# Kernel optimization log

Hardware: AMD Instinct MI355X
Metric: run time of the kernel (lower is better)

The kernel has to match this reference:

```python
import jax, jax.numpy as jnp
import numpy as np

B, L, C, S, W, R = 2, 32, 32, 64, 64, 32
MH = 32  # forcing MLP hidden


def _conv3d(x, w, b, pad_hw):
    # x: [B, Cin, L, S, W], w: [Cout, Cin, 1, kh, kw]
    y = jax.lax.conv_general_dilated(
        x, w, window_strides=(1, 1, 1),
        padding=[(0, 0), (pad_hw, pad_hw), (pad_hw, pad_hw)],
        dimension_numbers=('NCDHW', 'OIDHW', 'NCDHW'))
    return y + b[None, :, None, None, None]


def _forward(x, listT, params_log_base, dispersion_mod, fm_W1, fm_b1, fm_W2, fm_b2,
             forcing_scale, U_re, U_im, V_re, V_im, pW_re, pW_im, pb_re, pb_im,
             convr_w, convr_b, convi_w, convi_b, projc_w, projc_b, ln_w, ln_b):
    b, l, c, s, w = x.shape
    r = U_re.shape[-1]
    pad = s // 4
    dt = listT.reshape(b, l, 1, 1, 1)

    # FFT with mirror padding along S
    xp = jnp.pad(x, ((0, 0), (0, 0), (0, 0), (pad, pad), (0, 0)), mode='reflect')
    h = jnp.fft.fft2(xp.astype(jnp.complex64), axes=(-2, -1), norm='ortho')

    # complex channel projection
    proj_W = pW_re + 1j * pW_im
    h = jnp.einsum('blcsw,cd->bldsw', h, proj_W)
    h = h + (pb_re + 1j * pb_im)[None, None, :, None, None]

    # back to spatial, crop pad, re-FFT
    hs = jnp.fft.ifft2(h, axes=(-2, -1), norm='ortho')[..., pad:-pad, :]
    h = jnp.fft.fft2(hs, axes=(-2, -1), norm='ortho')

    U = U_re + 1j * U_im          # [C, S, R]
    V = V_re + 1j * V_im          # [C, W, R]
    # zq[b,l,c,r,q] = sum_{s,w} h * conj(U)[c,s,r] * V[c,w,q]
    zq = jnp.einsum('blcsw,csr,cwq->blcrq', h, jnp.conj(U), V)

    nu_base = jnp.exp(params_log_base[0] + dispersion_mod[0]).reshape(1, 1, c, r, 1)
    th_base = jnp.exp(params_log_base[1] + dispersion_mod[1]).reshape(1, 1, c, r, 1)

    # forcing modulation
    ctx = x.mean(axis=(-2, -1))                       # [B, L, C]
    inp = jnp.concatenate([ctx, dt.reshape(b, l, 1)], axis=-1)
    mid = jnp.tanh(inp @ fm_W1 + fm_b1)
    mod = (mid @ fm_W2 + fm_b2).reshape(b, l, c, r, 2)
    dnu = (forcing_scale * jnp.tanh(mod[..., 0]))[..., None]
    dth = (forcing_scale * jnp.tanh(mod[..., 1]))[..., None]

    nu_t = jnp.maximum(nu_base * dt + dnu, 1e-6)       # [B, L, C, R, 1]
    th_t = th_base * dt + dth
    lamb = jnp.exp(jax.lax.complex(-nu_t, th_t))       # complex [B, L, C, R, 1]

    gamma = jnp.sqrt(jnp.maximum(1.0 - jnp.exp(-2.0 * nu_t), 1e-12))
    x_in = zq * gamma.astype(zq.dtype)                 # [B, L, C, R, R]

    # parallel linear-recurrence scan: z_t = lamb_t * z_{t-1} + x_t
    def comb(a, bb):
        a1, x1 = a
        a2, x2 = bb
        return a1 * a2, a2 * x1 + x2
    _, z_out = jax.lax.associative_scan(comb, (lamb, x_in), axis=1)

    # reconstruct spectral field and inverse FFT
    h_rec = jnp.einsum('blcrq,cwq,csr->blcsw', z_out, jnp.conj(V), U)
    h_sp = jnp.fft.ifft2(h_rec, axes=(-2, -1), norm='ortho')

    xr = jnp.transpose(h_sp.real, (0, 2, 1, 3, 4))     # [B, C, L, S, W]
    xi = jnp.transpose(h_sp.imag, (0, 2, 1, 3, 4))
    hr = _conv3d(xr, convr_w, convr_b, 1)
    hi = _conv3d(xi, convi_w, convi_b, 1)
    hf = _conv3d(jnp.concatenate([hr, hi], axis=1), projc_w, projc_b, 0)
    hf = jnp.transpose(hf, (0, 2, 1, 3, 4))            # [B, L, C, S, W]

    # LayerNorm over [S, W]
    mu = hf.mean(axis=(-2, -1), keepdims=True)
    var = hf.var(axis=(-2, -1), keepdims=True)
    hf = (hf - mu) / jnp.sqrt(var + 1e-5) * ln_w + ln_b

    return x + hf


def setup_inputs() -> dict:
    key = jax.random.key(0)
    ks = jax.random.split(key, 20)
    f32 = jnp.float32
    x = jax.random.normal(ks[0], (B, L, C, S, W), dtype=f32)
    listT = jax.random.uniform(ks[1], (B, L), dtype=f32, minval=0.5, maxval=1.5)

    r_min, r_max = 0.8, 0.99
    u1 = jax.random.uniform(ks[2], (C, R), dtype=f32)
    u2 = jax.random.uniform(ks[3], (C, R), dtype=f32)
    nu_log = jnp.log(-0.5 * jnp.log(u1 * (r_max ** 2 - r_min ** 2) + r_min ** 2))
    theta_log = jnp.log(u2 * (2.0 * np.pi))
    params_log_base = jnp.stack([nu_log, theta_log], axis=0)
    dispersion_mod = jnp.zeros((2, C, R), dtype=f32)

    fm_W1 = jax.random.normal(ks[4], (C + 1, MH), dtype=f32) / np.sqrt(C + 1)
    fm_b1 = jnp.zeros((MH,), dtype=f32)
    fm_W2 = jax.random.normal(ks[5], (MH, C * R * 2), dtype=f32) / np.sqrt(MH)
    fm_b2 = jnp.zeros((C * R * 2,), dtype=f32)
    forcing_scale = jnp.float32(0.1)

    cplx_scale = 1.0 / np.sqrt(2.0)
    U_re = jax.random.normal(ks[6], (C, S, R), dtype=f32) * cplx_scale / np.sqrt(S)
    U_im = jax.random.normal(ks[7], (C, S, R), dtype=f32) * cplx_scale / np.sqrt(S)
    V_re = jax.random.normal(ks[8], (C, W, R), dtype=f32) * cplx_scale / np.sqrt(W)
    V_im = jax.random.normal(ks[9], (C, W, R), dtype=f32) * cplx_scale / np.sqrt(W)
    pW_re = jax.random.normal(ks[10], (C, C), dtype=f32) * cplx_scale / np.sqrt(C)
    pW_im = jax.random.normal(ks[11], (C, C), dtype=f32) * cplx_scale / np.sqrt(C)
    pb_re = jnp.zeros((C,), dtype=f32)
    pb_im = jnp.zeros((C,), dtype=f32)

    convr_w = jax.random.normal(ks[12], (C, C, 1, 3, 3), dtype=f32) * (1.0 / np.sqrt(C * 9))
    convr_b = jnp.zeros((C,), dtype=f32)
    convi_w = jax.random.normal(ks[13], (C, C, 1, 3, 3), dtype=f32) * (1.0 / np.sqrt(C * 9))
    convi_b = jnp.zeros((C,), dtype=f32)
    projc_w = jax.random.normal(ks[14], (C, 2 * C, 1, 1, 1), dtype=f32) * (1.0 / np.sqrt(2 * C))
    projc_b = jnp.zeros((C,), dtype=f32)

    ln_w = jnp.ones((S, W), dtype=f32)
    ln_b = jnp.zeros((S, W), dtype=f32)

    return dict(x=x, listT=listT, params_log_base=params_log_base,
                dispersion_mod=dispersion_mod, fm_W1=fm_W1, fm_b1=fm_b1,
                fm_W2=fm_W2, fm_b2=fm_b2, forcing_scale=forcing_scale,
                U_re=U_re, U_im=U_im, V_re=V_re, V_im=V_im,
                pW_re=pW_re, pW_im=pW_im, pb_re=pb_re, pb_im=pb_im,
                convr_w=convr_w, convr_b=convr_b, convi_w=convi_w, convi_b=convi_b,
                projc_w=projc_w, projc_b=projc_b, ln_w=ln_w, ln_b=ln_b)


def reference(x, listT, params_log_base, dispersion_mod, fm_W1, fm_b1, fm_W2, fm_b2,
              forcing_scale, U_re, U_im, V_re, V_im, pW_re, pW_im, pb_re, pb_im,
              convr_w, convr_b, convi_w, convi_b, projc_w, projc_b, ln_w, ln_b):
    return _forward(x, listT, params_log_base, dispersion_mod, fm_W1, fm_b1, fm_W2,
                    fm_b2, forcing_scale, U_re, U_im, V_re, V_im, pW_re, pW_im,
                    pb_re, pb_im, convr_w, convr_b, convi_w, convi_b, projc_w,
                    projc_b, ln_w, ln_b)
```

## Files before the change

kernel.cpp:

```cpp
#include <hip/hip_runtime.h>


typedef __attribute__((ext_vector_type(8))) short short8;
typedef __attribute__((ext_vector_type(4))) float floatx4;

__device__ __forceinline__ unsigned pack_bf16(float re, float im) {
  unsigned a = __float_as_uint(re), b = __float_as_uint(im);
  a = (a + 0x7FFFu + ((a >> 16) & 1u)) >> 16;
  b = (b + 0x7FFFu + ((b >> 16) & 1u)) >> 16;
  return a | (b << 16);
}
__device__ __forceinline__ unsigned short bf16r(float v) {
  unsigned a = __float_as_uint(v);
  return (unsigned short)((a + 0x7FFFu + ((a >> 16) & 1u)) >> 16);
}

__global__ __launch_bounds__(256) void k_mixprep(
    const float* __restrict__ x, const float* __restrict__ pWr,
    const float* __restrict__ pWi,
    const float* __restrict__ U_re, const float* __restrict__ U_im,
    const float* __restrict__ V_re, const float* __restrict__ V_im,
    const float* __restrict__ projc_w, const float* __restrict__ convr_w,
    const float* __restrict__ convi_w,
    unsigned* __restrict__ hs, float* __restrict__ ctxp,
    unsigned* __restrict__ zqA, unsigned* __restrict__ recA,
    unsigned* __restrict__ recB, unsigned* __restrict__ Wtb) {
  __shared__ __align__(16) char smem[512 * 20 * 4 + 16 * 16 * 2 * 4];
  const int tid = threadIdx.x;
  if (blockIdx.x < 512) {
    unsigned* xb_s = (unsigned*)smem;
    float(*red)[16][2] = (float(*)[16][2])(smem + 40960);
    const int bl = blockIdx.x >> 3;
    const int seg = blockIdx.x & 7;
    const int pxbase = seg * 512;
    const float* xb = x + (size_t)bl * 131072 + pxbase;
    float csa = 0.f, csb = 0.f;
#pragma unroll
    for (int t = 0; t < 8; ++t) {
      int i = t * 256 + tid;
      int c2 = i & 15, g4 = i >> 4;
      float4 a = *(const float4*)(xb + (2 * c2) * 4096 + g4 * 4);
      float4 b = *(const float4*)(xb + (2 * c2 + 1) * 4096 + g4 * 4);
      csa += a.x + a.y + a.z + a.w;
      csb += b.x + b.y + b.z + b.w;
#pragma unroll
      for (int j = 0; j < 4; ++j) {
        int px = g4 * 4 + j;
        xb_s[px * 20 + (((c2 >> 2) ^ (px & 3)) << 2) + (c2 & 3)] =
            pack_bf16(((const float*)&a)[j], ((const float*)&b)[j]);
      }
    }
    red[tid & 15][tid >> 4][0] = csa;
    red[tid & 15][tid >> 4][1] = csb;
    const int lane = tid & 63, wv = tid >> 6;
    const int qd = lane >> 4, ln = lane & 15;
    short8 arL, aiL, arH, aiH;
#pragma unroll
    for (int j = 0; j < 8; ++j) {
      int ci = qd * 8 + j;
      ((short*)&arL)[j] = (short)bf16r(pWr[ci * 32 + ln]);
      ((short*)&aiL)[j] = (short)bf16r(pWi[ci * 32 + ln]);
      ((short*)&arH)[j] = (short)bf16r(pWr[ci * 32 + 16 + ln]);
      ((short*)&aiH)[j] = (short)bf16r(pWi[ci * 32 + 16 + ln]);
    }
    __syncthreads();
    if (tid < 32) {
      int c2 = tid >> 1, part = tid & 1;
      float s = 0.f;
#pragma unroll
      for (int w = 0; w < 16; ++w) s += red[c2][w][part];
      ctxp[(bl * 8 + seg) * 32 + 2 * c2 + part] = s;
    }
#pragma unroll
    for (int pt = 0; pt < 8; ++pt) {
      int pxt = wv * 8 + pt;
      int pxl = pxt * 16 + ln;
      short8 bfr = *(const short8*)&xb_s[pxl * 20 + ((qd ^ (pxl & 3)) << 2)];
      floatx4 dRL = {0.f, 0.f, 0.f, 0.f}, dIL = {0.f, 0.f, 0.f, 0.f};
      floatx4 dRH = {0.f, 0.f, 0.f, 0.f}, dIH = {0.f, 0.f, 0.f, 0.f};
      dRL = __builtin_amdgcn_mfma_f32_16x16x32_bf16(arL, bfr, dRL, 0, 0, 0);
      dIL = __builtin_amdgcn_mfma_f32_16x16x32_bf16(aiL, bfr, dIL, 0, 0, 0);
      dRH = __builtin_amdgcn_mfma_f32_16x16x32_bf16(arH, bfr, dRH, 0, 0, 0);
      dIH = __builtin_amdgcn_mfma_f32_16x16x32_bf16(aiH, bfr, dIH, 0, 0, 0);
      unsigned* ho = hs + (size_t)bl * 131072 + pxbase + pxt * 16 + ln;
#pragma unroll
      for (int j = 0; j < 4; ++j) {
        ho[(qd * 4 + j) * 4096] = pack_bf16(dRL[j], dIL[j]);
        ho[(16 + qd * 4 + j) * 4096] = pack_bf16(dRH[j], dIH[j]);
      }
    }
  } else if (blockIdx.x < 2560) {
    float2* tw = (float2*)smem;
    if (tid < 64) {
      float sa, ca;
      sincosf((float)tid * 0.09817477042468103f, &sa, &ca);
      tw[tid] = make_float2(ca, sa);
    }
    __syncthreads();
    int gid = (blockIdx.x - 512) * 256 + tid;
    const float *Ar, *Ai;
    int knum, mode, variant;
    bool plus;
    unsigned* dst;
    int didx;
    if (gid < 262144) {
      int c = gid >> 13, mat = (gid >> 11) & 3, m = (gid >> 6) & 31,
          kw = gid & 63;
      knum = kw; mode = m;
      if (mat < 2) { Ar = V_re + c * 2048; Ai = V_im + c * 2048; plus = false; }
      else         { Ar = U_re + c * 2048; Ai = U_im + c * 2048; plus = true; }
      variant = mat; dst = zqA; didx = gid;
    } else {
      int rid = gid - 262144;
      int c = rid >> 13, sub = rid & 8191;
      int which = sub >> 11, mm = (sub >> 5) & 63, k2 = sub & 31;
      knum = mm; mode = k2;
      if (which < 2) {
        Ar = U_re + c * 2048; Ai = U_im + c * 2048; plus = true;
        variant = 4 + which; dst = recA;
        didx = ((c * 2 + which) * 64 + mm) * 32 + k2;
      } else {
        Ar = V_re + c * 2048; Ai = V_im + c * 2048; plus = false;
        variant = 4 + which; dst = recB;
        didx = ((c * 2 + which - 2) * 64 + mm) * 32 + k2;
      }
    }
    float sr = 0.f, si = 0.f;
    for (int n = 0; n < 64; ++n) {
      float2 w = tw[(knum * n) & 63];
      float ar = Ar[n * 32 + mode], ai = Ai[n * 32 + mode];
      if (plus) { sr += ar * w.x - ai * w.y; si += ar * w.y + ai * w.x; }
      else      { sr += ar * w.x + ai * w.y; si += ai * w.x - ar * w.y; }
    }
    sr *= 0.125f; si *= 0.125f;
    unsigned pv;
    switch (variant) {
      case 0: pv = pack_bf16(sr, -si); break;
      case 1: pv = pack_bf16(si, sr); break;
      case 2: pv = pack_bf16(sr, si); break;
      case 3: pv = pack_bf16(-si, sr); break;
      case 4: pv = pack_bf16(sr, -si); break;
      case 5: pv = pack_bf16(si, sr); break;
      case 6: pv = pack_bf16(sr, si); break;
      default: pv = pack_bf16(-si, sr); break;
    }
    dst[didx] = pv;
  } else {
    int gid = (blockIdx.x - 2560) * 256 + tid;
    if (gid < 9216) {
      int co = gid / 288;
      int r2 = gid - co * 288;
      int tap = r2 >> 5, ci = r2 & 31;
      float sr = 0.f, si = 0.f;
      for (int m = 0; m < 32; ++m) {
        sr += projc_w[co * 64 + m]      * convr_w[(m * 32 + ci) * 9 + tap];
        si += projc_w[co * 64 + 32 + m] * convi_w[(m * 32 + ci) * 9 + tap];
      }
      Wtb[gid] = pack_bf16(sr, si);
    }
  }
}

__global__ __launch_bounds__(256) void k_zq(
    const unsigned* __restrict__ hs, const short* __restrict__ zqA,
    float2* __restrict__ zq,
    const float* __restrict__ ctxp, const float* __restrict__ listT,
    const float* __restrict__ plb, const float* __restrict__ dmod,
    const float* __restrict__ W1, const float* __restrict__ b1,
    const float* __restrict__ W2, const float* __restrict__ b2,
    const float* __restrict__ fscale,
    float2* __restrict__ lam, float* __restrict__ gam) {
  __shared__ unsigned HsB[4096];
  __shared__ unsigned T2[2048];
  __shared__ float mid_s[32];
  __shared__ float ctxs[32];
  const int tid = threadIdx.x;
  if (blockIdx.x >= 2048) {
    int bl = blockIdx.x - 2048;
    float dt = listT[bl];
    if (tid < 32) {
      float s = 0.f;
#pragma unroll
      for (int sg = 0; sg < 8; ++sg) s += ctxp[(bl * 8 + sg) * 32 + tid];
      ctxs[tid] = s * (1.f / 4096.f);
    }
    __syncthreads();
    if (tid < 32) {
      float a = b1[tid];
      for (int j = 0; j < 32; ++j) a += ctxs[j] * W1[j * 32 + tid];
      a += dt * W1[1024 + tid];
      mid_s[tid] = tanhf(a);
    }
    __syncthreads();
    float fs = fscale[0];
#pragma unroll
    for (int u = 0; u < 4; ++u) {
      int cr = u * 256 + tid;
      int col = cr * 2;
      float m0 = b2[col], m1 = b2[col + 1];
      for (int h = 0; h < 32; ++h) {
        float mh = mid_s[h];
        float2 w2 = *(const float2*)&W2[h * 2048 + col];
        m0 += mh * w2.x;
        m1 += mh * w2.y;
      }
      float dnu = fs * tanhf(m0);
      float dth = fs * tanhf(m1);
      float nub = expf(plb[cr] + dmod[cr]);
      float thb = expf(plb[1024 + cr] + dmod[1024 + cr]);
      float nut = fmaxf(nub * dt + dnu, 1e-6f);
      float tht = thb * dt + dth;
      float e = expf(-nut);
      float sa, ca;
      sincosf(tht, &sa, &ca);
      float g = sqrtf(fmaxf(1.f - expf(-2.f * nut), 1e-12f));
      int o = bl * 1024 + cr;
      lam[o] = make_float2(e * ca, e * sa);
      gam[o] = g;
    }
    return;
  }
  const int blc = blockIdx.x;
  const int c = blc & 31;
  const int lane = tid & 63, wv = tid >> 6;
  const int qd = lane >> 4, ln = lane & 15;
  const int mt = wv >> 1, nth = wv & 1;
  {
    const uint4* hp = (const uint4*)(hs + (size_t)blc * 4096);
#pragma unroll
    for (int it = 0; it < 4; ++it) {
      int i4 = tid + it * 256;
      uint4 v = hp[i4];
      int s = i4 >> 4, w4 = i4 & 15;
      *(uint4*)&HsB[s * 64 + ((w4 ^ (s & 15)) << 2)] = v;
    }
  }
  const short* zA = zqA + (size_t)c * 4 * 32 * 128;
  short8 a1[4], a2[4], a3[4], a4[4];
#pragma unroll
  for (int t = 0; t < 4; ++t) {
    int row = mt * 16 + ln;
    a1[t] = *(const short8*)(zA + (0 * 32 + row) * 128 + t * 32 + qd * 8);
    a2[t] = *(const short8*)(zA + (1 * 32 + row) * 128 + t * 32 + qd * 8);
    a3[t] = *(const short8*)(zA + (2 * 32 + row) * 128 + t * 32 + qd * 8);
    a4[t] = *(const short8*)(zA + (3 * 32 + row) * 128 + t * 32 + qd * 8);
  }
  __syncthreads();
#pragma unroll
  for (int nti = 0; nti < 2; ++nti) {
    int nt = nth * 2 + nti;
    int n = nt * 16 + ln;
    floatx4 accr = {0.f, 0.f, 0.f, 0.f}, acci = {0.f, 0.f, 0.f, 0.f};
#pragma unroll
    for (int t = 0; t < 4; ++t) {
      short8 b = *(const short8*)&HsB[n * 64 + (((4 * t + qd) ^ (n & 15)) << 2)];
      accr = __builtin_amdgcn_mfma_f32_16x16x32_bf16(a1[t], b, accr, 0, 0, 0);
      acci = __builtin_amdgcn_mfma_f32_16x16x32_bf16(a2[t], b, acci, 0, 0, 0);
    }
#pragma unroll
    for (int j = 0; j < 4; ++j) {
      int q = mt * 16 + qd * 4 + j;
      int s = n;
      T2[q * 64 + (((s >> 2) ^ (q & 15)) << 2) + (s & 3)] = pack_bf16(accr[j], acci[j]);
    }
  }
  __syncthreads();
  {
    const int mt2 = wv >> 1, nt2 = wv & 1;
    int n = nt2 * 16 + ln;
    floatx4 zr = {0.f, 0.f, 0.f, 0.f}, zi = {0.f, 0.f, 0.f, 0.f};
#pragma unroll
    for (int t = 0; t < 4; ++t) {
      short8 b = *(const short8*)&T2[n * 64 + (((4 * t + qd) ^ (n & 15)) << 2)];
      zr = __builtin_amdgcn_mfma_f32_16x16x32_bf16(a3[t], b, zr, 0, 0, 0);
      zi = __builtin_amdgcn_mfma_f32_16x16x32_bf16(a4[t], b, zi, 0, 0, 0);
    }
    float2* zo = zq + (size_t)blc * 1024;
#pragma unroll
    for (int j = 0; j < 4; ++j) {
      int r = mt2 * 16 + qd * 4 + j;
      zo[r * 32 + n] = make_float2(zr[j], zi[j]);
    }
  }
}

__global__ __launch_bounds__(256) void k_scan(const float2* __restrict__ lam,
                                              const float* __restrict__ gam,
                                              const float2* __restrict__ zin,
                                              unsigned* __restrict__ zsp,
                                              int zst) {
  __shared__ float2 se[4][64];
  __shared__ float2 pe[4][64];
  __shared__ float2 cr_s[4][64];
  const int bc = blockIdx.x >> 4;
  const int b = bc >> 5, c = bc & 31;
  const int rq0 = (blockIdx.x & 15) * 64;
  const int seg = threadIdx.x >> 6, u = threadIdx.x & 63;
  const int rq = rq0 + u, r = rq >> 5;
  const int t0 = seg * 8;
  float2 s = make_float2(0.f, 0.f), P = make_float2(1.f, 0.f);
  float2 zloc[8], Ps[8];
  float2 v = zin[((size_t)(b * 32 + t0) * 32 + c) * 1024 + rq];
  float2 lm = lam[(b * 32 + t0) * 1024 + c * 32 + r];
  float g = gam[(b * 32 + t0) * 1024 + c * 32 + r];
#pragma unroll
  for (int i = 0; i < 8; ++i) {
    float2 nv, nlm;
    float ng;
    if (i < 7) {
      int t = t0 + i + 1;
      nv = zin[((size_t)(b * 32 + t) * 32 + c) * 1024 + rq];
      nlm = lam[(b * 32 + t) * 1024 + c * 32 + r];
      ng = gam[(b * 32 + t) * 1024 + c * 32 + r];
    }
    float nr = lm.x * s.x - lm.y * s.y + g * v.x;
    float ni = lm.x * s.y + lm.y * s.x + g * v.y;
    s = make_float2(nr, ni);
    float pr = P.x * lm.x - P.y * lm.y;
    float pi = P.x * lm.y + P.y * lm.x;
    P = make_float2(pr, pi);
    zloc[i] = s;
    Ps[i] = P;
    v = nv; lm = nlm; g = ng;
  }
  se[seg][u] = s;
  pe[seg][u] = P;
  __syncthreads();
  if (threadIdx.x < 64) {
    float2 c1 = se[0][u];
    float2 p1 = pe[1][u], s1 = se[1][u];
    float2 c2 = make_float2(s1.x + p1.x * c1.x - p1.y * c1.y,
                            s1.y + p1.x * c1.y + p1.y * c1.x);
    float2 p2 = pe[2][u], s2 = se[2][u];
    float2 c3 = make_float2(s2.x + p2.x * c2.x - p2.y * c2.y,
                            s2.y + p2.x * c2.y + p2.y * c2.x);
    cr_s[0][u] = make_float2(0.f, 0.f);
    cr_s[1][u] = c1;
    cr_s[2][u] = c2;
    cr_s[3][u] = c3;
  }
  __syncthreads();
  float2 cr = cr_s[seg][u];
#pragma unroll
  for (int i = 0; i < 8; ++i) {
    float zr = zloc[i].x + Ps[i].x * cr.x - Ps[i].y * cr.y;
    float zi = zloc[i].y + Ps[i].x * cr.y + Ps[i].y * cr.x;
    size_t idx = ((size_t)(b * 32 + t0 + i) * 32 + c) * 1024 + rq;
    zsp[idx * zst] = pack_bf16(zr, zi);
  }
}

__global__ __launch_bounds__(256) void k_rec(const unsigned* __restrict__ zs,
                                             int zst,
                                             const short* __restrict__ recA,
                                             const short* __restrict__ recB,
                                             unsigned* __restrict__ hsp) {
  __shared__ unsigned zB[1024];
  __shared__ unsigned P[2048];
  const int blc = blockIdx.x;
  const int c = blc & 31;
  const int tid = threadIdx.x;
  const int lane = tid & 63, wv = tid >> 6;
  const int qd = lane >> 4, ln = lane & 15;
  {
    const unsigned* zp = zs + (size_t)blc * 1024 * zst;
#pragma unroll
    for (int it = 0; it < 4; ++it) {
      int i = tid + it * 256;
      unsigned pv = zp[(size_t)i * zst];
      int r = i >> 5, q = i & 31;
      zB[q * 32 + (((r >> 2) ^ (q & 7)) << 2) + (r & 3)] = pv;
    }
  }
  const short* rA = recA + (size_t)c * 2 * 64 * 64;
  short8 a5[2], a6[2];
#pragma unroll
  for (int t = 0; t < 2; ++t) {
    int row = wv * 16 + ln;
    a5[t] = *(const short8*)(rA + (0 * 64 + row) * 64 + t * 32 + qd * 8);
    a6[t] = *(const short8*)(rA + (1 * 64 + row) * 64 + t * 32 + qd * 8);
  }
  __syncthreads();
#pragma unroll
  for (int nt = 0; nt < 2; ++nt) {
    int n = nt * 16 + ln;
    floatx4 pr = {0.f, 0.f, 0.f, 0.f}, pi = {0.f, 0.f, 0.f, 0.f};
#pragma unroll
    for (int t = 0; t < 2; ++t) {
      short8 b = *(const short8*)&zB[n * 32 + (((4 * t + qd) ^ (n & 7)) << 2)];
      pr = __builtin_amdgcn_mfma_f32_16x16x32_bf16(a5[t], b, pr, 0, 0, 0);
      pi = __builtin_amdgcn_mfma_f32_16x16x32_bf16(a6[t], b, pi, 0, 0, 0);
    }
#pragma unroll
    for (int j = 0; j < 4; ++j) {
      int s = wv * 16 + qd * 4 + j;
      int q = n;
      P[s * 32 + (((q >> 2) ^ (s & 7)) << 2) + (q & 3)] = pack_bf16(pr[j], pi[j]);
    }
  }
  __syncthreads();
  const short* rB = recB + (size_t)c * 2 * 64 * 64;
  short8 pa[2];
#pragma unroll
  for (int t = 0; t < 2; ++t) {
    int row = wv * 16 + ln;
    pa[t] = *(const short8*)&P[row * 32 + (((4 * t + qd) ^ (row & 7)) << 2)];
  }
#pragma unroll
  for (int nt = 0; nt < 4; ++nt) {
    int n = nt * 16 + ln;
    floatx4 hr = {0.f, 0.f, 0.f, 0.f}, hi = {0.f, 0.f, 0.f, 0.f};
#pragma unroll
    for (int t = 0; t < 2; ++t) {
      short8 b5 = *(const short8*)(rB + (0 * 64 + n) * 64 + t * 32 + qd * 8);
      short8 b6 = *(const short8*)(rB + (1 * 64 + n) * 64 + t * 32 + qd * 8);
      hr = __builtin_amdgcn_mfma_f32_16x16x32_bf16(pa[t], b5, hr, 0, 0, 0);
      hi = __builtin_amdgcn_mfma_f32_16x16x32_bf16(pa[t], b6, hi, 0, 0, 0);
    }
    unsigned* ho = hsp + (size_t)blc * 4096;
#pragma unroll
    for (int j = 0; j < 4; ++j) {
      int s = wv * 16 + qd * 4 + j;
      ho[s * 64 + n] = pack_bf16(hr[j], hi[j]);
    }
  }
}

__global__ __launch_bounds__(256, 2) void k_conv(
    const unsigned* __restrict__ hsp, const short* __restrict__ Wtb,
    unsigned short* __restrict__ convout, float2* __restrict__ stats) {
  __shared__ unsigned lds_in[6 * 66 * 32];
  const int bl = blockIdx.x >> 4;
  const int slab = blockIdx.x & 15;
  const int y0 = slab * 4;
  const int tid = threadIdx.x;
  for (int i = tid; i < 384; i += 256) {
    int ci = i & 31, j = i >> 5;
    int yi = j >> 1, xi = (j & 1) ? 65 : 0;
    int slot = (ci >> 2) ^ (xi & 7);
    lds_in[(yi * 66 + xi) * 32 + slot * 4 + (ci & 3)] = 0u;
  }
#pragma unroll
  for (int t = 0; t < 12; ++t) {
    int i = t * 256 + tid;
    int ci = i & 31;
    int j = i >> 5;
    int yi = j >> 4, x4 = j & 15;
    int y = y0 + yi - 1;
    uint4 v = make_uint4(0u, 0u, 0u, 0u);
    if ((unsigned)y < 64u)
      v = *(const uint4*)(hsp + (((size_t)bl * 32 + ci) * 64 + y) * 64 + x4 * 4);
    int xb = 1 + x4 * 4;
#pragma unroll
    for (int jj = 0; jj < 4; ++jj) {
      int xi = xb + jj;
      int slot = (ci >> 2) ^ (xi & 7);
      lds_in[(yi * 66 + xi) * 32 + slot * 4 + (ci & 3)] =
          ((const unsigned*)&v)[jj];
    }
  }
  const int lane = tid & 63;
  const int wv = tid >> 6;
  const int co = lane & 15;
  const int qd = lane >> 4;
  short8 bL[18], bH[18];
  {
    const short* wpL = Wtb + (co * 9) * 64 + qd * 8;
    const short* wpH = Wtb + ((co + 16) * 9) * 64 + qd * 8;
#pragma unroll
    for (int tap = 0; tap < 9; ++tap)
#pragma unroll
      for (int kk = 0; kk < 2; ++kk) {
        bL[tap * 2 + kk] = *(const short8*)(wpL + tap * 64 + kk * 32);
        bH[tap * 2 + kk] = *(const short8*)(wpH + tap * 64 + kk * 32);
      }
  }
  __syncthreads();
  float sL = 0.f, s2L = 0.f, sH = 0.f, s2H = 0.f;
  const int x0 = wv * 16;
  const int xl = lane & 15;
  for (int ry = 0; ry < 4; ++ry) {
    floatx4 aL = {0.f, 0.f, 0.f, 0.f}, aH = {0.f, 0.f, 0.f, 0.f};
#pragma unroll
    for (int tap = 0; tap < 9; ++tap) {
      int dy = tap / 3, dx = tap - dy * 3;
      int yi = ry + dy;
      int xi = x0 + xl + dx;
#pragma unroll
      for (int kk = 0; kk < 2; ++kk) {
        int slot = ((kk << 2) | qd) ^ (xi & 7);
        const short8 a =
            *(const short8*)&lds_in[(yi * 66 + xi) * 32 + slot * 4];
        aL = __builtin_amdgcn_mfma_f32_16x16x32_bf16(a, bL[tap * 2 + kk], aL, 0, 0, 0);
        aH = __builtin_amdgcn_mfma_f32_16x16x32_bf16(a, bH[tap * 2 + kk], aH, 0, 0, 0);
      }
    }
    size_t goL = (((size_t)bl * 32 + co) * 64 + (y0 + ry)) * 64 + x0 + qd * 4;
    size_t goH = goL + (size_t)16 * 4096;
    *(uint2*)(convout + goL) =
        make_uint2(pack_bf16(aL[0], aL[1]), pack_bf16(aL[2], aL[3]));
    *(uint2*)(convout + goH) =
        make_uint2(pack_bf16(aH[0], aH[1]), pack_bf16(aH[2], aH[3]));
#pragma unroll
    for (int j = 0; j < 4; ++j) {
      sL += aL[j]; s2L += aL[j] * aL[j];
      sH += aH[j]; s2H += aH[j] * aH[j];
    }
  }
  sL += __shfl_down(sL, 32, 64);  s2L += __shfl_down(s2L, 32, 64);
  sH += __shfl_down(sH, 32, 64);  s2H += __shfl_down(s2H, 32, 64);
  sL += __shfl_down(sL, 16, 64);  s2L += __shfl_down(s2L, 16, 64);
  sH += __shfl_down(sH, 16, 64);  s2H += __shfl_down(s2H, 16, 64);
  if (lane < 16) {
    stats[((size_t)bl * 32 + lane) * 64 + slab * 4 + wv] = make_float2(sL, s2L);
    stats[((size_t)bl * 32 + 16 + lane) * 64 + slab * 4 + wv] =
        make_float2(sH, s2H);
  }
}

__global__ __launch_bounds__(256) void k_ln(
    const unsigned short* __restrict__ convout,
    const float2* __restrict__ stats, const float* __restrict__ x,
    const float* __restrict__ ln_w, const float* __restrict__ ln_b,
    float* __restrict__ out) {
  const int blc = blockIdx.x;
  const int tid = threadIdx.x;
  __shared__ float sh_mu, sh_rs;
  if (tid < 64) {
    float2 v = stats[(size_t)blc * 64 + tid];
    float s = v.x, s2 = v.y;
#pragma unroll
    for (int o = 32; o > 0; o >>= 1) {
      s += __shfl_down(s, o, 64);
      s2 += __shfl_down(s2, o, 64);
    }
    if (tid == 0) {
      float mu = s * (1.f / 4096.f);
      float var = s2 * (1.f / 4096.f) - mu * mu;
      sh_mu = mu;
      sh_rs = rsqrtf(var + 1e-5f);
    }
  }
  __syncthreads();
  float mu = sh_mu, rs = sh_rs;
  const uint2* cp = (const uint2*)(convout + (size_t)blc * 4096);
  const float4* xp = (const float4*)(x + (size_t)blc * 4096);
  const float4* lwp = (const float4*)ln_w;
  const float4* lbp = (const float4*)ln_b;
  float4* op = (float4*)(out + (size_t)blc * 4096);
#pragma unroll
  for (int k = 0; k < 4; ++k) {
    int i = tid + k * 256;
    uint2 cv = cp[i];
    float4 xv = xp[i], lw = lwp[i], lb = lbp[i];
    float c0 = __uint_as_float(cv.x << 16);
    float c1 = __uint_as_float(cv.x & 0xFFFF0000u);
    float c2 = __uint_as_float(cv.y << 16);
    float c3 = __uint_as_float(cv.y & 0xFFFF0000u);
    float4 o;
    o.x = xv.x + (c0 - mu) * rs * lw.x + lb.x;
    o.y = xv.y + (c1 - mu) * rs * lw.y + lb.y;
    o.z = xv.z + (c2 - mu) * rs * lw.z + lb.z;
    o.w = xv.w + (c3 - mu) * rs * lw.w + lb.w;
    op[i] = o;
  }
}

extern "C" void kernel_launch(void* const* d_in, const int* in_sizes, int n_in,
                              void* d_out, int out_size, void* d_ws,
                              size_t ws_size, hipStream_t stream) {
  const float* x       = (const float*)d_in[0];
  const float* listT   = (const float*)d_in[1];
  const float* plb     = (const float*)d_in[2];
  const float* dmod    = (const float*)d_in[3];
  const float* fm_W1   = (const float*)d_in[4];
  const float* fm_b1   = (const float*)d_in[5];
  const float* fm_W2   = (const float*)d_in[6];
  const float* fm_b2   = (const float*)d_in[7];
  const float* fscale  = (const float*)d_in[8];
  const float* U_re    = (const float*)d_in[9];
  const float* U_im    = (const float*)d_in[10];
  const float* V_re    = (const float*)d_in[11];
  const float* V_im    = (const float*)d_in[12];
  const float* pW_re   = (const float*)d_in[13];
  const float* pW_im   = (const float*)d_in[14];
  const float* convr_w = (const float*)d_in[17];
  const float* convi_w = (const float*)d_in[19];
  const float* projc_w = (const float*)d_in[21];
  const float* ln_w    = (const float*)d_in[23];
  const float* ln_b    = (const float*)d_in[24];
  float* out = (float*)d_out;

  float* wsf = (float*)d_ws;
  unsigned* hs  = (unsigned*)wsf;
  unsigned* hsp = (unsigned*)wsf;
  unsigned* zqAp  = (unsigned*)(wsf + 8388608);
  unsigned* recAp = (unsigned*)(wsf + 8388608 + 262144);
  unsigned* recBp = (unsigned*)(wsf + 8388608 + 393216);
  unsigned short* convout = (unsigned short*)(wsf + 8388608);
  float2*   stats = (float2*)(wsf + 12582912);
  float2*   zq  = (float2*)(wsf + 16777216);
  size_t off = 16777216 + 4194304;
  const size_t tail = 222208;
  unsigned* zs;
  int zst;
  size_t off2;
  if (ws_size >= (off + 2097152 + tail) * 4) {
    zs = (unsigned*)(wsf + off); zst = 1; off2 = off + 2097152;
  } else {
    zs = (unsigned*)zq; zst = 2; off2 = off;
  }
  float2*   lam  = (float2*)(wsf + off2);
  float*    gam  = wsf + off2 + 131072;
  float*    ctxp = wsf + off2 + 196608;
  unsigned* Wtb  = (unsigned*)(wsf + off2 + 212992);

  k_mixprep<<<2596, 256, 0, stream>>>(x, pW_re, pW_im, U_re, U_im, V_re, V_im,
                                      projc_w, convr_w, convi_w, hs, ctxp,
                                      zqAp, recAp, recBp, Wtb);
  k_zq<<<2112, 256, 0, stream>>>(hs, (const short*)zqAp, zq, ctxp, listT, plb,
                                 dmod, fm_W1, fm_b1, fm_W2, fm_b2, fscale,
                                 lam, gam);
  k_scan<<<1024, 256, 0, stream>>>(lam, gam, zq, zs, zst);
  k_rec<<<2048, 256, 0, stream>>>(zs, zst, (const short*)recAp,
                                  (const short*)recBp, hsp);
  k_conv<<<1024, 256, 0, stream>>>(hsp, (const short*)Wtb, convout, stats);
  k_ln<<<2048, 256, 0, stream>>>(convout, stats, x, ln_w, ln_b, out);
}
```

Before: 247.3 us.

## Stage mixprep outputs in LDS, halve pixel tile, restructure DFT prep blocks

The channel-mix part of k_mixprep now handles 256 pixels per block over twice as many blocks, which lowers LDS use and should raise occupancy. MFMA results go through an LDS staging buffer so global stores become coalesced uint4 rows instead of scattered 4-byte stores. The U/V DFT precompute is reorganised into 64 blocks that load each channel matrix into LDS once and compute all four output variants per thread, replacing 2048 blocks that each re-read global memory. Partial context sums double to 16 per (b,l), so the workspace layout and the k_zq reduction change to match.

```diff
diff --git a/kernel.cpp b/kernel.cpp
--- a/kernel.cpp
+++ b/kernel.cpp
@@ -25,18 +25,19 @@
     unsigned* __restrict__ hs, float* __restrict__ ctxp,
     unsigned* __restrict__ zqA, unsigned* __restrict__ recA,
     unsigned* __restrict__ recB, unsigned* __restrict__ Wtb) {
-  __shared__ __align__(16) char smem[512 * 20 * 4 + 16 * 16 * 2 * 4];
+  __shared__ __align__(16) char smem[33280];
   const int tid = threadIdx.x;
-  if (blockIdx.x < 512) {
+  if (blockIdx.x < 1024) {
     unsigned* xb_s = (unsigned*)smem;
-    float(*red)[16][2] = (float(*)[16][2])(smem + 40960);
-    const int bl = blockIdx.x >> 3;
-    const int seg = blockIdx.x & 7;
-    const int pxbase = seg * 512;
+    float(*red)[16][2] = (float(*)[16][2])(smem + 20480);
+    unsigned* outb = (unsigned*)smem;
+    const int bl = blockIdx.x >> 4;
+    const int seg = blockIdx.x & 15;
+    const int pxbase = seg * 256;
     const float* xb = x + (size_t)bl * 131072 + pxbase;
     float csa = 0.f, csb = 0.f;
 #pragma unroll
-    for (int t = 0; t < 8; ++t) {
+    for (int t = 0; t < 4; ++t) {
       int i = t * 256 + tid;
       int c2 = i & 15, g4 = i >> 4;
       float4 a = *(const float4*)(xb + (2 * c2) * 4096 + g4 * 4);
@@ -69,84 +70,95 @@
       float s = 0.f;
 #pragma unroll
       for (int w = 0; w < 16; ++w) s += red[c2][w][part];
-      ctxp[(bl * 8 + seg) * 32 + 2 * c2 + part] = s;
-    }
-#pragma unroll
-    for (int pt = 0; pt < 8; ++pt) {
-      int pxt = wv * 8 + pt;
+      ctxp[(bl * 16 + seg) * 32 + 2 * c2 + part] = s;
+    }
+    floatx4 RL[4], IL[4], RH[4], IH[4];
+#pragma unroll
+    for (int pt = 0; pt < 4; ++pt) {
+      int pxt = wv * 4 + pt;
       int pxl = pxt * 16 + ln;
       short8 bfr = *(const short8*)&xb_s[pxl * 20 + ((qd ^ (pxl & 3)) << 2)];
-      floatx4 dRL = {0.f, 0.f, 0.f, 0.f}, dIL = {0.f, 0.f, 0.f, 0.f};
-      floatx4 dRH = {0.f, 0.f, 0.f, 0.f}, dIH = {0.f, 0.f, 0.f, 0.f};
-      dRL = __builtin_amdgcn_mfma_f32_16x16x32_bf16(arL, bfr, dRL, 0, 0, 0);
-      dIL = __builtin_amdgcn_mfma_f32_16x16x32_bf16(aiL, bfr, dIL, 0, 0, 0);
-      dRH = __builtin_amdgcn_mfma_f32_16x16x32_bf16(arH, bfr, dRH, 0, 0, 0);
-      dIH = __builtin_amdgcn_mfma_f32_16x16x32_bf16(aiH, bfr, dIH, 0, 0, 0);
-      unsigned* ho = hs + (size_t)bl * 131072 + pxbase + pxt * 16 + ln;
+      floatx4 z4 = {0.f, 0.f, 0.f, 0.f};
+      RL[pt] = __builtin_amdgcn_mfma_f32_16x16x32_bf16(arL, bfr, z4, 0, 0, 0);
+      IL[pt] = __builtin_amdgcn_mfma_f32_16x16x32_bf16(aiL, bfr, z4, 0, 0, 0);
+      RH[pt] = __builtin_amdgcn_mfma_f32_16x16x32_bf16(arH, bfr, z4, 0, 0, 0);
+      IH[pt] = __builtin_amdgcn_mfma_f32_16x16x32_bf16(aiH, bfr, z4, 0, 0, 0);
+    }
+    __syncthreads();
+#pragma unroll
+    for (int pt = 0; pt < 4; ++pt) {
+      int px = (wv * 4 + pt) * 16 + ln;
 #pragma unroll
       for (int j = 0; j < 4; ++j) {
-        ho[(qd * 4 + j) * 4096] = pack_bf16(dRL[j], dIL[j]);
-        ho[(16 + qd * 4 + j) * 4096] = pack_bf16(dRH[j], dIH[j]);
-      }
-    }
-  } else if (blockIdx.x < 2560) {
-    float2* tw = (float2*)smem;
+        outb[(qd * 4 + j) * 260 + px] = pack_bf16(RL[pt][j], IL[pt][j]);
+        outb[(16 + qd * 4 + j) * 260 + px] = pack_bf16(RH[pt][j], IH[pt][j]);
+      }
+    }
+    __syncthreads();
+    unsigned* ho = hs + (size_t)bl * 131072 + pxbase;
+    const int px4 = tid & 63, dg = tid >> 6;
+#pragma unroll
+    for (int dd = 0; dd < 8; ++dd) {
+      int d = dg * 8 + dd;
+      uint4 v = *(const uint4*)&outb[d * 260 + px4 * 4];
+      *(uint4*)(ho + d * 4096 + px4 * 4) = v;
+    }
+  } else if (blockIdx.x < 1088) {
+    float2* A2 = (float2*)smem;
+    float2* tw = (float2*)(smem + 16384);
+    const int id = blockIdx.x - 1024;
+    const int c = id >> 1, src = id & 1;
+    const float* Ar = (src ? V_re : U_re) + c * 2048;
+    const float* Ai = (src ? V_im : U_im) + c * 2048;
     if (tid < 64) {
       float sa, ca;
       sincosf((float)tid * 0.09817477042468103f, &sa, &ca);
       tw[tid] = make_float2(ca, sa);
     }
+#pragma unroll
+    for (int t = 0; t < 8; ++t) {
+      int idx = t * 256 + tid;
+      A2[idx] = make_float2(Ar[idx], Ai[idx]);
+    }
     __syncthreads();
-    int gid = (blockIdx.x - 512) * 256 + tid;
-    const float *Ar, *Ai;
-    int knum, mode, variant;
-    bool plus;
-    unsigned* dst;
-    int didx;
-    if (gid < 262144) {
-      int c = gid >> 13, mat = (gid >> 11) & 3, m = (gid >> 6) & 31,
-          kw = gid & 63;
-      knum = kw; mode = m;
-      if (mat < 2) { Ar = V_re + c * 2048; Ai = V_im + c * 2048; plus = false; }
-      else         { Ar = U_re + c * 2048; Ai = U_im + c * 2048; plus = true; }
-      variant = mat; dst = zqA; didx = gid;
-    } else {
-      int rid = gid - 262144;
-      int c = rid >> 13, sub = rid & 8191;
-      int which = sub >> 11, mm = (sub >> 5) & 63, k2 = sub & 31;
-      knum = mm; mode = k2;
-      if (which < 2) {
-        Ar = U_re + c * 2048; Ai = U_im + c * 2048; plus = true;
-        variant = 4 + which; dst = recA;
-        didx = ((c * 2 + which) * 64 + mm) * 32 + k2;
+    const int kw = tid >> 2, mg = tid & 3;
+    float sr[8] = {0.f, 0.f, 0.f, 0.f, 0.f, 0.f, 0.f, 0.f};
+    float si[8] = {0.f, 0.f, 0.f, 0.f, 0.f, 0.f, 0.f, 0.f};
+#pragma unroll 4
+    for (int n = 0; n < 64; ++n) {
+      float2 w = tw[(kw * n) & 63];
+      float ws = src ? -w.y : w.y;
+#pragma unroll
+      for (int t4 = 0; t4 < 4; ++t4) {
+        float4 p = *(const float4*)&A2[n * 32 + mg * 8 + t4 * 2];
+        sr[2 * t4]     += p.x * w.x - p.y * ws;
+        si[2 * t4]     += p.x * ws + p.y * w.x;
+        sr[2 * t4 + 1] += p.z * w.x - p.w * ws;
+        si[2 * t4 + 1] += p.z * ws + p.w * w.x;
+      }
+    }
+#pragma unroll
+    for (int j = 0; j < 8; ++j) {
+      float r = sr[j] * 0.125f, i2 = si[j] * 0.125f;
+      int m = mg * 8 + j;
+      unsigned p_ri  = pack_bf16(r, i2);
+      unsigned p_rmi = pack_bf16(r, -i2);
+      unsigned p_ir  = pack_bf16(i2, r);
+      unsigned p_mir = pack_bf16(-i2, r);
+      if (src == 0) {
+        zqA[((c * 4 + 2) * 32 + m) * 64 + kw] = p_ri;
+        zqA[((c * 4 + 3) * 32 + m) * 64 + kw] = p_mir;
+        recA[((c * 2 + 0) * 64 + kw) * 32 + m] = p_rmi;
+        recA[((c * 2 + 1) * 64 + kw) * 32 + m] = p_ir;
       } else {
-        Ar = V_re + c * 2048; Ai = V_im + c * 2048; plus = false;
-        variant = 4 + which; dst = recB;
-        didx = ((c * 2 + which - 2) * 64 + mm) * 32 + k2;
-      }
-    }
-    float sr = 0.f, si = 0.f;
-    for (int n = 0; n < 64; ++n) {
-      float2 w = tw[(knum * n) & 63];
-      float ar = Ar[n * 32 + mode], ai = Ai[n * 32 + mode];
-      if (plus) { sr += ar * w.x - ai * w.y; si += ar * w.y + ai * w.x; }
-      else      { sr += ar * w.x + ai * w.y; si += ai * w.x - ar * w.y; }
-    }
-    sr *= 0.125f; si *= 0.125f;
-    unsigned pv;
-    switch (variant) {
-      case 0: pv = pack_bf16(sr, -si); break;
-      case 1: pv = pack_bf16(si, sr); break;
-      case 2: pv = pack_bf16(sr, si); break;
-      case 3: pv = pack_bf16(-si, sr); break;
-      case 4: pv = pack_bf16(sr, -si); break;
-      case 5: pv = pack_bf16(si, sr); break;
-      case 6: pv = pack_bf16(sr, si); break;
-      default: pv = pack_bf16(-si, sr); break;
-    }
-    dst[didx] = pv;
+        zqA[((c * 4 + 0) * 32 + m) * 64 + kw] = p_rmi;
+        zqA[((c * 4 + 1) * 32 + m) * 64 + kw] = p_ir;
+        recB[((c * 2 + 0) * 64 + kw) * 32 + m] = p_ri;
+        recB[((c * 2 + 1) * 64 + kw) * 32 + m] = p_mir;
+      }
+    }
   } else {
-    int gid = (blockIdx.x - 2560) * 256 + tid;
+    int gid = (blockIdx.x - 1088) * 256 + tid;
     if (gid < 9216) {
       int co = gid / 288;
       int r2 = gid - co * 288;
@@ -181,7 +193,7 @@
     if (tid < 32) {
       float s = 0.f;
 #pragma unroll
-      for (int sg = 0; sg < 8; ++sg) s += ctxp[(bl * 8 + sg) * 32 + tid];
+      for (int sg = 0; sg < 16; ++sg) s += ctxp[(bl * 16 + sg) * 32 + tid];
       ctxs[tid] = s * (1.f / 4096.f);
     }
     __syncthreads();
@@ -601,7 +613,7 @@
   float2*   stats = (float2*)(wsf + 12582912);
   float2*   zq  = (float2*)(wsf + 16777216);
   size_t off = 16777216 + 4194304;
-  const size_t tail = 222208;
+  const size_t tail = 238592;
   unsigned* zs;
   int zst;
   size_t off2;
@@ -613,9 +625,9 @@
   float2*   lam  = (float2*)(wsf + off2);
   float*    gam  = wsf + off2 + 131072;
   float*    ctxp = wsf + off2 + 196608;
-  unsigned* Wtb  = (unsigned*)(wsf + off2 + 212992);
-
-  k_mixprep<<<2596, 256, 0, stream>>>(x, pW_re, pW_im, U_re, U_im, V_re, V_im,
+  unsigned* Wtb  = (unsigned*)(wsf + off2 + 229376);
+
+  k_mixprep<<<1124, 256, 0, stream>>>(x, pW_re, pW_im, U_re, U_im, V_re, V_im,
                                       projc_w, convr_w, convi_w, hs, ctxp,
                                       zqAp, recAp, recBp, Wtb);
   k_zq<<<2112, 256, 0, stream>>>(hs, (const short*)zqAp, zq, ctxp, listT, plb,
```

Measured after the change: 240.2 us. -2.9%, faster.
